# Kernel optimization log

Hardware: AMD Instinct MI355X
Metric: run time of the kernel (lower is better)

The kernel has to match this reference:

```python
import jax, jax.numpy as jnp
import numpy as np

B, NQ, S, D = 8, 1024, 2048, 512

def setup_inputs() -> dict:
    key = jax.random.key(0)
    k1, k2, k3, k4 = jax.random.split(key, 4)
    queries = jax.random.normal(k1, (B, NQ, D), dtype=jnp.float32)
    keys = jax.random.normal(k2, (B, S, D), dtype=jnp.float32)
    values = jax.random.normal(k3, (B, S, D), dtype=jnp.float32)
    mask = jax.random.randint(k4, (B, NQ, S), 0, 2, dtype=jnp.int32)
    return {"queries": queries, "keys": keys, "values": values, "mask": mask}

def reference(queries, keys, values, mask):
    # scores: dot-product attention scores (b, nq, s)
    scores = jnp.einsum('bqd,bsd->bqs', queries, keys)
    attention_dist = jax.nn.softmax(scores, axis=2)
    # mask then renormalize over seq axis
    attention_dist = attention_dist * mask.astype(attention_dist.dtype)
    attention_dist = attention_dist / attention_dist.sum(axis=2, keepdims=True)
    # weighted sum of values: equivalent to (dist.unsqueeze(3) * values.unsqueeze(1)).sum(2)
    final_vector = jnp.einsum('bqs,bsd->bqd', attention_dist, values)
    return final_vector
```

## Files before the change

### kernel.cpp

```cpp
#include <hip/hip_runtime.h>


#define Bz 8
#define NQz 1024
#define Sz 2048
#define Dz 512
#define QT 32
#define TS 32
#define NT ((Sz / 2) / TS)
#define KP 520
#define PP 40

typedef _Float16 f16x8 __attribute__((ext_vector_type(8)));
typedef float f32x4 __attribute__((ext_vector_type(4)));
typedef unsigned short ushort_t;

#define AS1(p) ((const __attribute__((address_space(1))) unsigned int*)(p))
#define AS3(p) ((__attribute__((address_space(3))) unsigned int*)(p))
#define DRAIN_ALL() __builtin_amdgcn_s_waitcnt(0)

__device__ __forceinline__ ushort_t f2h(float x) {
  _Float16 h = (_Float16)x;
  return __builtin_bit_cast(ushort_t, h);
}
__device__ __forceinline__ float h2f(ushort_t u) {
  return (float)__builtin_bit_cast(_Float16, u);
}

__global__ __launch_bounds__(256)
void prep(const float* __restrict__ K, const float* __restrict__ V,
          const int* __restrict__ Mi, ushort_t* __restrict__ Kf,
          ushort_t* __restrict__ Vt, unsigned* __restrict__ Mp) {
  __shared__ ushort_t sT[64][41];
  const int t = threadIdx.x;
  int bx = blockIdx.x;
  if (bx < 8192) {
    size_t e = ((size_t)bx * 256 + t) * 4;
    float4 v = *(const float4*)(K + e);
    uint2 w;
    w.x = (unsigned)f2h(v.x) | ((unsigned)f2h(v.y) << 16);
    w.y = (unsigned)f2h(v.z) | ((unsigned)f2h(v.w) << 16);
    *(uint2*)(Kf + e) = w;
    return;
  }
  bx -= 8192;
  if (bx < 4096) {
    const int b = bx >> 9;
    const int rest = bx & 511;
    const int st = rest >> 4;
    const int dt = rest & 15;
    const int s0 = st * 64, d0 = dt * 32;
    const float* Vb = V + ((size_t)b * Sz + s0) * Dz + d0;
#pragma unroll
    for (int i = 0; i < 2; ++i) {
      int idx = t + 256 * i;
      int s = idx >> 3;
      int dc = (idx & 7) * 4;
      float4 v = *(const float4*)(Vb + (size_t)s * Dz + dc);
      uint2 w;
      w.x = (unsigned)f2h(v.x) | ((unsigned)f2h(v.y) << 16);
      w.y = (unsigned)f2h(v.z) | ((unsigned)f2h(v.w) << 16);
      *(uint2*)(&sT[s][dc]) = w;
    }
    __syncthreads();
    ushort_t* VtB = Vt + ((size_t)b * Dz + d0) * Sz + s0;
    int d = t >> 3, c = t & 7;
    uint4 u;
    ushort_t* tp = (ushort_t*)&u;
#pragma unroll
    for (int j = 0; j < 8; ++j) tp[j] = sT[c * 8 + j][d];
    *(uint4*)(VtB + (size_t)d * Sz + c * 8) = u;
    return;
  }
  bx -= 4096;
  const int lane = t & 63;
  const size_t base = (size_t)bx * 1024 + t * 4;
  const int4 mv = *(const int4*)(Mi + base);
  unsigned nib = (mv.x ? 1u : 0u) | (mv.y ? 2u : 0u) |
                 (mv.z ? 4u : 0u) | (mv.w ? 8u : 0u);
  unsigned v = nib << ((lane & 7) * 4);
  v |= __shfl_xor(v, 1);
  v |= __shfl_xor(v, 2);
  v |= __shfl_xor(v, 4);
  if ((lane & 7) == 0) Mp[bx * 32 + (t >> 3)] = v;
}

__global__ __launch_bounds__(256, 2)
void attn_flash(const float* __restrict__ Q, const unsigned* __restrict__ Mp,
                const ushort_t* __restrict__ Kf, const ushort_t* __restrict__ Vt,
                float* __restrict__ Opart, float* __restrict__ Mpart,
                float* __restrict__ Lpart) {
  __shared__ ushort_t sK[TS][KP];
  __shared__ ushort_t sV[Dz][TS];
  __shared__ ushort_t sP[QT][PP];
  __shared__ float sTMax[2][QT];
  __shared__ float sTSum[2][QT];
  __shared__ float sM[2][QT];
  __shared__ float sL[2][QT];

  const int tid  = threadIdx.x;
  const int wave = tid >> 6;
  const int lane = tid & 63;
  const int l16  = lane & 15;
  const int quad = lane >> 4;
  const int rw   = wave & 1;
  const int cw   = wave >> 1;

  int bxr = blockIdx.x;
  const int bx = (bxr & 7) * 64 + (bxr >> 3);
  const int b  = bx >> 6;
  const int r6 = bx & 63;
  const int qt = r6 >> 1;
  const int sh = r6 & 1;
  const int q0 = qt * QT;
  const int sbeg = sh * (Sz / 2);

  const float*    Qb  = Q  + ((size_t)b * NQz + q0) * Dz;
  const ushort_t* KfB = Kf + (size_t)b * Sz * Dz;
  const ushort_t* VtB = Vt + (size_t)b * Dz * Sz;
  const unsigned* MpB = Mp + ((size_t)b * NQz + q0) * (Sz / 32);

  auto issue_k = [&](int s0n) {
#pragma unroll
    for (int j = 0; j < 8; ++j) {
      int row = wave * 8 + j;
      const ushort_t* gp = KfB + (size_t)(s0n + row) * Dz + lane * 8;
      __builtin_amdgcn_global_load_lds(AS1(gp), AS3(&sK[row][0]), 16, 0, 0);
    }
  };
  auto issue_v = [&](int s0n) {
#pragma unroll
    for (int j = 0; j < 8; ++j) {
      int dbase = wave * 128 + j * 16;
      const ushort_t* gp =
          VtB + (size_t)(dbase + (lane >> 2)) * Sz + s0n + (lane & 3) * 8;
      __builtin_amdgcn_global_load_lds(AS1(gp), AS3(&sV[dbase][0]), 16, 0, 0);
    }
  };
  auto load_mask = [&](int s0n) -> unsigned {
    return MpB[(size_t)(rw * 16 + l16) * (Sz / 32) + (s0n >> 5)];
  };

  issue_k(sbeg);
  unsigned msk_cur = load_mask(sbeg);

  f16x8 qa[16];
  {
    const float* qrow = Qb + (size_t)(rw * 16 + l16) * Dz;
#pragma unroll
    for (int kk = 0; kk < 16; ++kk) {
      const float4 a = *(const float4*)(qrow + kk * 32 + quad * 8);
      const float4 c = *(const float4*)(qrow + kk * 32 + quad * 8 + 4);
      f16x8 h;
      h[0] = (_Float16)a.x; h[1] = (_Float16)a.y;
      h[2] = (_Float16)a.z; h[3] = (_Float16)a.w;
      h[4] = (_Float16)c.x; h[5] = (_Float16)c.y;
      h[6] = (_Float16)c.z; h[7] = (_Float16)c.w;
      qa[kk] = h;
    }
  }

  if (tid < QT) { sM[0][tid] = -1e30f; sL[0][tid] = 0.0f; }

  f32x4 oacc[16];
#pragma unroll
  for (int t = 0; t < 16; ++t) oacc[t] = (f32x4){0.f, 0.f, 0.f, 0.f};

  int p = 0;
  for (int i = 0; i < NT; ++i) {
    const int s0 = sbeg + i * TS;
    const int sNext = (i + 1 < NT) ? s0 + TS : sbeg;

    DRAIN_ALL();
    __syncthreads();

    issue_v(s0);

    f32x4 sc0 = (f32x4){0.f, 0.f, 0.f, 0.f};
    f32x4 sc1 = (f32x4){0.f, 0.f, 0.f, 0.f};
    {
      const ushort_t* kh = &sK[cw * 16 + l16][quad * 8];
#pragma unroll
      for (int kk = 0; kk < 16; kk += 2) {
        f16x8 b0 = *(const f16x8*)(kh + kk * 32);
        f16x8 b1 = *(const f16x8*)(kh + kk * 32 + 32);
        sc0 = __builtin_amdgcn_mfma_f32_16x16x32_f16(b0, qa[kk], sc0, 0, 0, 0);
        sc1 = __builtin_amdgcn_mfma_f32_16x16x32_f16(b1, qa[kk + 1], sc1, 0, 0, 0);
      }
    }
    f32x4 sc;
#pragma unroll
    for (int r = 0; r < 4; ++r) sc[r] = sc0[r] + sc1[r];

    const unsigned mbits = msk_cur >> (cw * 16 + quad * 4);
    float se[4];
#pragma unroll
    for (int r = 0; r < 4; ++r) se[r] = ((mbits >> r) & 1u) ? sc[r] : -1e30f;
    float rmax = fmaxf(fmaxf(se[0], se[1]), fmaxf(se[2], se[3]));
    rmax = fmaxf(rmax, __shfl_xor(rmax, 16));
    rmax = fmaxf(rmax, __shfl_xor(rmax, 32));
    ushort_t pb[4];
    float rsum = 0.f;
#pragma unroll
    for (int r = 0; r < 4; ++r) {
      float pv = ((mbits >> r) & 1u) ? __expf(se[r] - rmax) : 0.0f;
      pb[r] = f2h(pv);
      rsum += h2f(pb[r]);
    }
    {
      uint2 w;
      w.x = (unsigned)pb[0] | ((unsigned)pb[1] << 16);
      w.y = (unsigned)pb[2] | ((unsigned)pb[3] << 16);
      *(uint2*)(&sP[rw * 16 + l16][cw * 16 + quad * 4]) = w;
    }
    rsum += __shfl_xor(rsum, 16);
    rsum += __shfl_xor(rsum, 32);
    if (quad == 0) {
      sTMax[cw][rw * 16 + l16] = rmax;
      sTSum[cw][rw * 16 + l16] = rsum;
    }

    DRAIN_ALL();
    __syncthreads();

    issue_k(sNext);
    unsigned msk_nxt = load_mask(sNext);

    const int pr = p;
    f16x8 pa;
    {
      const int row16 = rw * 16 + l16;
      float t0v = sTMax[0][row16], t1v = sTMax[1][row16];
      float mo16 = sM[pr][row16];
      float mn16 = fmaxf(mo16, fmaxf(t0v, t1v));
      float scl = __expf(((quad >> 1) ? t1v : t0v) - mn16);
      f16x8 praw = *(const f16x8*)(&sP[row16][quad * 8]);
      _Float16 sh16 = (_Float16)scl;
#pragma unroll
      for (int j = 0; j < 8; ++j) pa[j] = praw[j] * sh16;
    }

    float dd[4];
    bool grow = false;
#pragma unroll
    for (int r = 0; r < 4; ++r) {
      const int rc = rw * 16 + quad * 4 + r;
      float a0 = sTMax[0][rc], a1 = sTMax[1][rc];
      float mo = sM[pr][rc];
      float mn = fmaxf(mo, fmaxf(a0, a1));
      dd[r] = mo - mn;
      grow = grow || (mn > mo);
      if (cw == 0 && l16 == 0) {
        sM[pr ^ 1][rc] = mn;
        sL[pr ^ 1][rc] = __expf(mo - mn) * sL[pr][rc]
                       + __expf(a0 - mn) * sTSum[0][rc]
                       + __expf(a1 - mn) * sTSum[1][rc];
      }
    }
    if (__any((int)grow)) {
      float al[4];
#pragma unroll
      for (int r = 0; r < 4; ++r) al[r] = __expf(dd[r]);
#pragma unroll
      for (int t = 0; t < 16; ++t)
#pragma unroll
        for (int r = 0; r < 4; ++r) oacc[t][r] *= al[r];
    }

#pragma unroll
    for (int t = 0; t < 16; ++t) {
      f16x8 vb = *(const f16x8*)(&sV[cw * 256 + t * 16 + l16][quad * 8]);
      oacc[t] = __builtin_amdgcn_mfma_f32_16x16x32_f16(pa, vb, oacc[t], 0, 0, 0);
    }

    msk_cur = msk_nxt;
    p ^= 1;
  }

  DRAIN_ALL();
  __syncthreads();
  const size_t rbase = (size_t)(b * 2 + sh) * NQz + q0;
#pragma unroll
  for (int t = 0; t < 16; ++t) {
#pragma unroll
    for (int r = 0; r < 4; ++r) {
      int rowq = rw * 16 + quad * 4 + r;
      Opart[(rbase + rowq) * Dz + cw * 256 + t * 16 + l16] = oacc[t][r];
    }
  }
  if (tid < QT) {
    Mpart[rbase + tid] = sM[p][tid];
    Lpart[rbase + tid] = sL[p][tid];
  }
}

__global__ __launch_bounds__(256)
void combine(const float* __restrict__ Opart, const float* __restrict__ Mpart,
             const float* __restrict__ Lpart, float* __restrict__ Out) {
  int gid = blockIdx.x * 256 + threadIdx.x;
  int row = gid >> 7;
  int b   = row >> 10;
  int q   = row & 1023;
  int c   = (gid & 127) * 4;
  size_t i0 = (size_t)(b * 2 + 0) * NQz + q;
  size_t i1 = (size_t)(b * 2 + 1) * NQz + q;
  float m0 = Mpart[i0], m1 = Mpart[i1];
  float l0 = Lpart[i0], l1 = Lpart[i1];
  float m  = fmaxf(m0, m1);
  float w0 = __expf(m0 - m), w1 = __expf(m1 - m);
  float inv = 1.0f / (w0 * l0 + w1 * l1);
  float4 a = *(const float4*)(Opart + i0 * Dz + c);
  float4 bv = *(const float4*)(Opart + i1 * Dz + c);
  float4 o;
  o.x = (w0 * a.x + w1 * bv.x) * inv;
  o.y = (w0 * a.y + w1 * bv.y) * inv;
  o.z = (w0 * a.z + w1 * bv.z) * inv;
  o.w = (w0 * a.w + w1 * bv.w) * inv;
  *(float4*)(Out + ((size_t)b * NQz + q) * Dz + c) = o;
}

extern "C" void kernel_launch(void* const* d_in, const int* in_sizes, int n_in,
                              void* d_out, int out_size, void* d_ws, size_t ws_size,
                              hipStream_t stream) {
  const float* Q = (const float*)d_in[0];
  const float* K = (const float*)d_in[1];
  const float* V = (const float*)d_in[2];
  const int*   M = (const int*)d_in[3];
  float* O = (float*)d_out;

  const size_t NKV = (size_t)Bz * Sz * Dz;
  ushort_t* Kf = (ushort_t*)d_ws;
  ushort_t* Vt = Kf + NKV;
  float* Opart = (float*)(Vt + NKV);
  float* Mpart = Opart + (size_t)Bz * 2 * NQz * Dz;
  float* Lpart = Mpart + (size_t)Bz * 2 * NQz;
  unsigned* Mp = (unsigned*)(Lpart + (size_t)Bz * 2 * NQz);

  prep<<<dim3(28672), dim3(256), 0, stream>>>(K, V, M, Kf, Vt, Mp);
  attn_flash<<<dim3(512), dim3(256), 0, stream>>>(Q, Mp, Kf, Vt, Opart, Mpart, Lpart);
  combine<<<dim3(4096), dim3(256), 0, stream>>>(Opart, Mpart, Lpart, O);
}
```

Baseline: 265.5 us.

## Restructure flash attention to 128-query tiles with per-wave rows and double-buffered K/V

The attention kernel now uses 512-thread blocks covering 128 queries, where each wave owns 16 query rows across the full D. This removes the cross-wave softmax reduction through shared memory and lets each K/V tile be reused by 8 waves instead of 2. K/V tiles are double-buffered with one barrier per step, the V shared layout is XOR-swizzled, and the sequence split becomes a template parameter (4 when workspace allows) with fp16 partial outputs to cut combine traffic. The costs are 128 accumulator registers per lane, which may hurt occupancy, and extra precision loss from fp16 partials.

```diff
diff --git a/kernel.cpp b/kernel.cpp
--- a/kernel.cpp
+++ b/kernel.cpp
@@ -5,9 +5,8 @@
 #define NQz 1024
 #define Sz 2048
 #define Dz 512
-#define QT 32
+#define QTT 128
 #define TS 32
-#define NT ((Sz / 2) / TS)
 #define KP 520
 #define PP 40
 
@@ -85,68 +84,66 @@
   if ((lane & 7) == 0) Mp[bx * 32 + (t >> 3)] = v;
 }
 
-__global__ __launch_bounds__(256, 2)
+template <int SPLIT>
+__global__ __launch_bounds__(512, 2)
 void attn_flash(const float* __restrict__ Q, const unsigned* __restrict__ Mp,
                 const ushort_t* __restrict__ Kf, const ushort_t* __restrict__ Vt,
-                float* __restrict__ Opart, float* __restrict__ Mpart,
+                ushort_t* __restrict__ Opart, float* __restrict__ Mpart,
                 float* __restrict__ Lpart) {
-  __shared__ ushort_t sK[TS][KP];
-  __shared__ ushort_t sV[Dz][TS];
-  __shared__ ushort_t sP[QT][PP];
-  __shared__ float sTMax[2][QT];
-  __shared__ float sTSum[2][QT];
-  __shared__ float sM[2][QT];
-  __shared__ float sL[2][QT];
+  __shared__ ushort_t sK[2][TS][KP];
+  __shared__ ushort_t sV[2][Dz][TS];
+  __shared__ ushort_t sP[8][16][PP];
 
   const int tid  = threadIdx.x;
   const int wave = tid >> 6;
   const int lane = tid & 63;
   const int l16  = lane & 15;
   const int quad = lane >> 4;
-  const int rw   = wave & 1;
-  const int cw   = wave >> 1;
-
-  int bxr = blockIdx.x;
-  const int bx = (bxr & 7) * 64 + (bxr >> 3);
-  const int b  = bx >> 6;
-  const int r6 = bx & 63;
-  const int qt = r6 >> 1;
-  const int sh = r6 & 1;
-  const int q0 = qt * QT;
-  const int sbeg = sh * (Sz / 2);
-
-  const float*    Qb  = Q  + ((size_t)b * NQz + q0) * Dz;
+
+  const int bxr = blockIdx.x;
+  const int b   = bxr & 7;
+  const int rest = bxr >> 3;
+  const int qt  = rest / SPLIT;
+  const int sh  = rest % SPLIT;
+  const int q0  = qt * QTT;
+  const int SLEN = Sz / SPLIT;
+  const int NTt  = SLEN / TS;
+  const int sbeg = sh * SLEN;
+  const int qw   = q0 + wave * 16;
+
+  const float*    Qb  = Q  + ((size_t)b * NQz + qw) * Dz;
   const ushort_t* KfB = Kf + (size_t)b * Sz * Dz;
   const ushort_t* VtB = Vt + (size_t)b * Dz * Sz;
-  const unsigned* MpB = Mp + ((size_t)b * NQz + q0) * (Sz / 32);
-
-  auto issue_k = [&](int s0n) {
-#pragma unroll
-    for (int j = 0; j < 8; ++j) {
-      int row = wave * 8 + j;
+  const unsigned* MpB = Mp + ((size_t)b * NQz + qw) * (Sz / 32);
+
+  const int vql  = (lane & 3) ^ ((lane >> 3) & 3);
+  const int vcol = (quad ^ ((l16 >> 1) & 3)) * 8;
+
+  auto issue_tile = [&](int s0n, int bsel) {
+#pragma unroll
+    for (int j = 0; j < 4; ++j) {
+      int row = wave * 4 + j;
       const ushort_t* gp = KfB + (size_t)(s0n + row) * Dz + lane * 8;
-      __builtin_amdgcn_global_load_lds(AS1(gp), AS3(&sK[row][0]), 16, 0, 0);
-    }
-  };
-  auto issue_v = [&](int s0n) {
-#pragma unroll
-    for (int j = 0; j < 8; ++j) {
-      int dbase = wave * 128 + j * 16;
-      const ushort_t* gp =
-          VtB + (size_t)(dbase + (lane >> 2)) * Sz + s0n + (lane & 3) * 8;
-      __builtin_amdgcn_global_load_lds(AS1(gp), AS3(&sV[dbase][0]), 16, 0, 0);
+      __builtin_amdgcn_global_load_lds(AS1(gp), AS3(&sK[bsel][row][0]), 16, 0, 0);
+    }
+#pragma unroll
+    for (int j = 0; j < 4; ++j) {
+      int dbase = wave * 64 + j * 16;
+      int d = dbase + (lane >> 2);
+      const ushort_t* gp = VtB + (size_t)d * Sz + s0n + vql * 8;
+      __builtin_amdgcn_global_load_lds(AS1(gp), AS3(&sV[bsel][dbase][0]), 16, 0, 0);
     }
   };
   auto load_mask = [&](int s0n) -> unsigned {
-    return MpB[(size_t)(rw * 16 + l16) * (Sz / 32) + (s0n >> 5)];
+    return MpB[(size_t)l16 * (Sz / 32) + (s0n >> 5)];
   };
 
-  issue_k(sbeg);
+  issue_tile(sbeg, 0);
   unsigned msk_cur = load_mask(sbeg);
 
   f16x8 qa[16];
   {
-    const float* qrow = Qb + (size_t)(rw * 16 + l16) * Dz;
+    const float* qrow = Qb + (size_t)l16 * Dz;
 #pragma unroll
     for (int kk = 0; kk < 16; ++kk) {
       const float4 a = *(const float4*)(qrow + kk * 32 + quad * 8);
@@ -159,163 +156,167 @@
       qa[kk] = h;
     }
   }
-
-  if (tid < QT) { sM[0][tid] = -1e30f; sL[0][tid] = 0.0f; }
-
-  f32x4 oacc[16];
-#pragma unroll
-  for (int t = 0; t < 16; ++t) oacc[t] = (f32x4){0.f, 0.f, 0.f, 0.f};
-
-  int p = 0;
-  for (int i = 0; i < NT; ++i) {
-    const int s0 = sbeg + i * TS;
-    const int sNext = (i + 1 < NT) ? s0 + TS : sbeg;
-
-    DRAIN_ALL();
-    __syncthreads();
-
-    issue_v(s0);
-
-    f32x4 sc0 = (f32x4){0.f, 0.f, 0.f, 0.f};
-    f32x4 sc1 = (f32x4){0.f, 0.f, 0.f, 0.f};
+  if (NTt > 1) issue_tile(sbeg + TS, 1);
+  DRAIN_ALL();
+  __syncthreads();
+
+  float m_ln = -1e30f, l_ln = 0.0f;
+  f32x4 oacc[32];
+#pragma unroll
+  for (int nt = 0; nt < 32; ++nt) oacc[nt] = (f32x4){0.f, 0.f, 0.f, 0.f};
+
+  const ushort_t* vbase0 = &sV[0][0][0] + (size_t)l16 * TS + vcol;
+  const ushort_t* vbase1 = &sV[1][0][0] + (size_t)l16 * TS + vcol;
+
+  for (int i = 0; i < NTt; ++i) {
+    const int buf = i & 1;
+    if (i) {
+      DRAIN_ALL();
+      __syncthreads();
+      if (i + 1 < NTt) issue_tile(sbeg + (i + 1) * TS, buf ^ 1);
+    }
+    unsigned msk_nxt = (i + 1 < NTt) ? load_mask(sbeg + (i + 1) * TS) : 0u;
+
+    f32x4 a00 = (f32x4){0.f,0.f,0.f,0.f}, a01 = (f32x4){0.f,0.f,0.f,0.f};
+    f32x4 a10 = (f32x4){0.f,0.f,0.f,0.f}, a11 = (f32x4){0.f,0.f,0.f,0.f};
     {
-      const ushort_t* kh = &sK[cw * 16 + l16][quad * 8];
+      const ushort_t* kh0 = &sK[buf][l16][quad * 8];
+      const ushort_t* kh1 = &sK[buf][16 + l16][quad * 8];
 #pragma unroll
       for (int kk = 0; kk < 16; kk += 2) {
-        f16x8 b0 = *(const f16x8*)(kh + kk * 32);
-        f16x8 b1 = *(const f16x8*)(kh + kk * 32 + 32);
-        sc0 = __builtin_amdgcn_mfma_f32_16x16x32_f16(b0, qa[kk], sc0, 0, 0, 0);
-        sc1 = __builtin_amdgcn_mfma_f32_16x16x32_f16(b1, qa[kk + 1], sc1, 0, 0, 0);
+        f16x8 k00 = *(const f16x8*)(kh0 + kk * 32);
+        f16x8 k10 = *(const f16x8*)(kh1 + kk * 32);
+        f16x8 k01 = *(const f16x8*)(kh0 + kk * 32 + 32);
+        f16x8 k11 = *(const f16x8*)(kh1 + kk * 32 + 32);
+        a00 = __builtin_amdgcn_mfma_f32_16x16x32_f16(k00, qa[kk], a00, 0, 0, 0);
+        a10 = __builtin_amdgcn_mfma_f32_16x16x32_f16(k10, qa[kk], a10, 0, 0, 0);
+        a01 = __builtin_amdgcn_mfma_f32_16x16x32_f16(k01, qa[kk+1], a01, 0, 0, 0);
+        a11 = __builtin_amdgcn_mfma_f32_16x16x32_f16(k11, qa[kk+1], a11, 0, 0, 0);
       }
     }
-    f32x4 sc;
-#pragma unroll
-    for (int r = 0; r < 4; ++r) sc[r] = sc0[r] + sc1[r];
-
-    const unsigned mbits = msk_cur >> (cw * 16 + quad * 4);
-    float se[4];
-#pragma unroll
-    for (int r = 0; r < 4; ++r) se[r] = ((mbits >> r) & 1u) ? sc[r] : -1e30f;
-    float rmax = fmaxf(fmaxf(se[0], se[1]), fmaxf(se[2], se[3]));
+    f32x4 s0v, s1v;
+#pragma unroll
+    for (int r = 0; r < 4; ++r) { s0v[r] = a00[r] + a01[r]; s1v[r] = a10[r] + a11[r]; }
+
+    const unsigned mb = msk_cur;
+    float se0[4], se1[4];
+#pragma unroll
+    for (int r = 0; r < 4; ++r) {
+      se0[r] = ((mb >> (quad * 4 + r)) & 1u)      ? s0v[r] : -1e30f;
+      se1[r] = ((mb >> (16 + quad * 4 + r)) & 1u) ? s1v[r] : -1e30f;
+    }
+    float rmax = fmaxf(fmaxf(fmaxf(se0[0], se0[1]), fmaxf(se0[2], se0[3])),
+                       fmaxf(fmaxf(se1[0], se1[1]), fmaxf(se1[2], se1[3])));
     rmax = fmaxf(rmax, __shfl_xor(rmax, 16));
     rmax = fmaxf(rmax, __shfl_xor(rmax, 32));
-    ushort_t pb[4];
+
+    ushort_t pb0[4], pb1[4];
     float rsum = 0.f;
 #pragma unroll
     for (int r = 0; r < 4; ++r) {
-      float pv = ((mbits >> r) & 1u) ? __expf(se[r] - rmax) : 0.0f;
-      pb[r] = f2h(pv);
-      rsum += h2f(pb[r]);
+      float p0 = ((mb >> (quad * 4 + r)) & 1u)      ? __expf(se0[r] - rmax) : 0.f;
+      float p1 = ((mb >> (16 + quad * 4 + r)) & 1u) ? __expf(se1[r] - rmax) : 0.f;
+      pb0[r] = f2h(p0); pb1[r] = f2h(p1);
+      rsum += h2f(pb0[r]) + h2f(pb1[r]);
     }
     {
-      uint2 w;
-      w.x = (unsigned)pb[0] | ((unsigned)pb[1] << 16);
-      w.y = (unsigned)pb[2] | ((unsigned)pb[3] << 16);
-      *(uint2*)(&sP[rw * 16 + l16][cw * 16 + quad * 4]) = w;
+      uint2 w0, w1;
+      w0.x = (unsigned)pb0[0] | ((unsigned)pb0[1] << 16);
+      w0.y = (unsigned)pb0[2] | ((unsigned)pb0[3] << 16);
+      w1.x = (unsigned)pb1[0] | ((unsigned)pb1[1] << 16);
+      w1.y = (unsigned)pb1[2] | ((unsigned)pb1[3] << 16);
+      *(uint2*)(&sP[wave][l16][quad * 4]) = w0;
+      *(uint2*)(&sP[wave][l16][16 + quad * 4]) = w1;
     }
     rsum += __shfl_xor(rsum, 16);
     rsum += __shfl_xor(rsum, 32);
-    if (quad == 0) {
-      sTMax[cw][rw * 16 + l16] = rmax;
-      sTSum[cw][rw * 16 + l16] = rsum;
-    }
-
-    DRAIN_ALL();
-    __syncthreads();
-
-    issue_k(sNext);
-    unsigned msk_nxt = load_mask(sNext);
-
-    const int pr = p;
+
+    float m_new = fmaxf(m_ln, rmax);
+    float scl   = __expf(rmax - m_new);
+    float al_ln = __expf(m_ln - m_new);
+    bool  grw   = m_new > m_ln;
+    l_ln = al_ln * l_ln + scl * rsum;
+    m_ln = m_new;
+
+    f16x8 praw = *(const f16x8*)(&sP[wave][l16][quad * 8]);
     f16x8 pa;
     {
-      const int row16 = rw * 16 + l16;
-      float t0v = sTMax[0][row16], t1v = sTMax[1][row16];
-      float mo16 = sM[pr][row16];
-      float mn16 = fmaxf(mo16, fmaxf(t0v, t1v));
-      float scl = __expf(((quad >> 1) ? t1v : t0v) - mn16);
-      f16x8 praw = *(const f16x8*)(&sP[row16][quad * 8]);
       _Float16 sh16 = (_Float16)scl;
 #pragma unroll
       for (int j = 0; j < 8; ++j) pa[j] = praw[j] * sh16;
     }
 
-    float dd[4];
-    bool grow = false;
+    if (__any((int)grw)) {
+      float al[4];
+#pragma unroll
+      for (int r = 0; r < 4; ++r) al[r] = __shfl(al_ln, quad * 4 + r);
+#pragma unroll
+      for (int nt = 0; nt < 32; ++nt)
+#pragma unroll
+        for (int r = 0; r < 4; ++r) oacc[nt][r] *= al[r];
+    }
+
+    const ushort_t* vb_ = buf ? vbase1 : vbase0;
+#pragma unroll
+    for (int nt = 0; nt < 32; ++nt) {
+      f16x8 vb = *(const f16x8*)(vb_ + nt * 512);
+      oacc[nt] = __builtin_amdgcn_mfma_f32_16x16x32_f16(pa, vb, oacc[nt], 0, 0, 0);
+    }
+
+    msk_cur = msk_nxt;
+  }
+
+  const size_t rbase = (size_t)(b * SPLIT + sh) * NQz + q0 + wave * 16;
+#pragma unroll
+  for (int nt = 0; nt < 32; ++nt) {
 #pragma unroll
     for (int r = 0; r < 4; ++r) {
-      const int rc = rw * 16 + quad * 4 + r;
-      float a0 = sTMax[0][rc], a1 = sTMax[1][rc];
-      float mo = sM[pr][rc];
-      float mn = fmaxf(mo, fmaxf(a0, a1));
-      dd[r] = mo - mn;
-      grow = grow || (mn > mo);
-      if (cw == 0 && l16 == 0) {
-        sM[pr ^ 1][rc] = mn;
-        sL[pr ^ 1][rc] = __expf(mo - mn) * sL[pr][rc]
-                       + __expf(a0 - mn) * sTSum[0][rc]
-                       + __expf(a1 - mn) * sTSum[1][rc];
-      }
-    }
-    if (__any((int)grow)) {
-      float al[4];
-#pragma unroll
-      for (int r = 0; r < 4; ++r) al[r] = __expf(dd[r]);
-#pragma unroll
-      for (int t = 0; t < 16; ++t)
-#pragma unroll
-        for (int r = 0; r < 4; ++r) oacc[t][r] *= al[r];
-    }
-
-#pragma unroll
-    for (int t = 0; t < 16; ++t) {
-      f16x8 vb = *(const f16x8*)(&sV[cw * 256 + t * 16 + l16][quad * 8]);
-      oacc[t] = __builtin_amdgcn_mfma_f32_16x16x32_f16(pa, vb, oacc[t], 0, 0, 0);
-    }
-
-    msk_cur = msk_nxt;
-    p ^= 1;
-  }
-
-  DRAIN_ALL();
-  __syncthreads();
-  const size_t rbase = (size_t)(b * 2 + sh) * NQz + q0;
-#pragma unroll
-  for (int t = 0; t < 16; ++t) {
-#pragma unroll
-    for (int r = 0; r < 4; ++r) {
-      int rowq = rw * 16 + quad * 4 + r;
-      Opart[(rbase + rowq) * Dz + cw * 256 + t * 16 + l16] = oacc[t][r];
-    }
-  }
-  if (tid < QT) {
-    Mpart[rbase + tid] = sM[p][tid];
-    Lpart[rbase + tid] = sL[p][tid];
-  }
-}
-
+      Opart[(rbase + quad * 4 + r) * Dz + nt * 16 + l16] = f2h(oacc[nt][r]);
+    }
+  }
+  if (quad == 0) {
+    Mpart[rbase + l16] = m_ln;
+    Lpart[rbase + l16] = l_ln;
+  }
+}
+
+template <int SPLIT>
 __global__ __launch_bounds__(256)
-void combine(const float* __restrict__ Opart, const float* __restrict__ Mpart,
+void combine(const ushort_t* __restrict__ Opart, const float* __restrict__ Mpart,
              const float* __restrict__ Lpart, float* __restrict__ Out) {
   int gid = blockIdx.x * 256 + threadIdx.x;
   int row = gid >> 7;
   int b   = row >> 10;
   int q   = row & 1023;
   int c   = (gid & 127) * 4;
-  size_t i0 = (size_t)(b * 2 + 0) * NQz + q;
-  size_t i1 = (size_t)(b * 2 + 1) * NQz + q;
-  float m0 = Mpart[i0], m1 = Mpart[i1];
-  float l0 = Lpart[i0], l1 = Lpart[i1];
-  float m  = fmaxf(m0, m1);
-  float w0 = __expf(m0 - m), w1 = __expf(m1 - m);
-  float inv = 1.0f / (w0 * l0 + w1 * l1);
-  float4 a = *(const float4*)(Opart + i0 * Dz + c);
-  float4 bv = *(const float4*)(Opart + i1 * Dz + c);
-  float4 o;
-  o.x = (w0 * a.x + w1 * bv.x) * inv;
-  o.y = (w0 * a.y + w1 * bv.y) * inv;
-  o.z = (w0 * a.z + w1 * bv.z) * inv;
-  o.w = (w0 * a.w + w1 * bv.w) * inv;
+  float mv[SPLIT], lv[SPLIT];
+  float m = -1e30f;
+#pragma unroll
+  for (int p = 0; p < SPLIT; ++p) {
+    size_t ip = (size_t)(b * SPLIT + p) * NQz + q;
+    mv[p] = Mpart[ip];
+    lv[p] = Lpart[ip];
+    m = fmaxf(m, mv[p]);
+  }
+  float w[SPLIT], denom = 0.f;
+#pragma unroll
+  for (int p = 0; p < SPLIT; ++p) {
+    w[p] = __expf(mv[p] - m);
+    denom += w[p] * lv[p];
+  }
+  float inv = 1.0f / denom;
+  float4 o = {0.f, 0.f, 0.f, 0.f};
+#pragma unroll
+  for (int p = 0; p < SPLIT; ++p) {
+    size_t ip = (size_t)(b * SPLIT + p) * NQz + q;
+    const ushort_t* op = Opart + ip * Dz + c;
+    uint2 raw = *(const uint2*)op;
+    o.x += w[p] * h2f((ushort_t)(raw.x & 0xffff));
+    o.y += w[p] * h2f((ushort_t)(raw.x >> 16));
+    o.z += w[p] * h2f((ushort_t)(raw.y & 0xffff));
+    o.w += w[p] * h2f((ushort_t)(raw.y >> 16));
+  }
+  o.x *= inv; o.y *= inv; o.z *= inv; o.w *= inv;
   *(float4*)(Out + ((size_t)b * NQz + q) * Dz + c) = o;
 }
 
@@ -328,15 +329,35 @@
   const int*   M = (const int*)d_in[3];
   float* O = (float*)d_out;
 
-  const size_t NKV = (size_t)Bz * Sz * Dz;
+  const size_t NKV   = (size_t)Bz * Sz * Dz;
+  const size_t maskW = (size_t)Bz * NQz * (Sz / 32);
+
   ushort_t* Kf = (ushort_t*)d_ws;
   ushort_t* Vt = Kf + NKV;
-  float* Opart = (float*)(Vt + NKV);
-  float* Mpart = Opart + (size_t)Bz * 2 * NQz * Dz;
-  float* Lpart = Mpart + (size_t)Bz * 2 * NQz;
-  unsigned* Mp = (unsigned*)(Lpart + (size_t)Bz * 2 * NQz);
+  unsigned* Mp = (unsigned*)(Vt + NKV);
+  ushort_t* Opart = (ushort_t*)(Mp + maskW);
+
+  auto need_bytes = [&](int S) -> size_t {
+    return NKV * 2 * 2 + maskW * 4
+         + (size_t)Bz * S * NQz * Dz * 2
+         + (size_t)Bz * S * NQz * 4 * 2;
+  };
 
   prep<<<dim3(28672), dim3(256), 0, stream>>>(K, V, M, Kf, Vt, Mp);
-  attn_flash<<<dim3(512), dim3(256), 0, stream>>>(Q, Mp, Kf, Vt, Opart, Mpart, Lpart);
-  combine<<<dim3(4096), dim3(256), 0, stream>>>(Opart, Mpart, Lpart, O);
-}
+
+  if (ws_size >= need_bytes(4)) {
+    constexpr int S = 4;
+    float* Mpart = (float*)(Opart + (size_t)Bz * S * NQz * Dz);
+    float* Lpart = Mpart + (size_t)Bz * S * NQz;
+    attn_flash<S><<<dim3(8 * (NQz / QTT) * S), dim3(512), 0, stream>>>(
+        Q, Mp, Kf, Vt, Opart, Mpart, Lpart);
+    combine<S><<<dim3(4096), dim3(256), 0, stream>>>(Opart, Mpart, Lpart, O);
+  } else {
+    constexpr int S = 2;
+    float* Mpart = (float*)(Opart + (size_t)Bz * S * NQz * Dz);
+    float* Lpart = Mpart + (size_t)Bz * S * NQz;
+    attn_flash<S><<<dim3(8 * (NQz / QTT) * S), dim3(512), 0, stream>>>(
+        Q, Mp, Kf, Vt, Opart, Mpart, Lpart);
+    combine<S><<<dim3(4096), dim3(256), 0, stream>>>(Opart, Mpart, Lpart, O);
+  }
+}
```

After: 246.7 us. -7.1%, faster.
